# Optimization experiments

Hardware: AMD Instinct MI355X
Metric: run time of the kernel (lower is better)

## Reference

```python
import jax, jax.numpy as jnp
import numpy as np

TAU = 1.0   # temperature
BETA = 1.0  # instance_alingment_weight


def setup_inputs() -> dict:
    key = jax.random.key(0)
    k1, k2, k3 = jax.random.split(key, 3)
    N, D = 1024, 128
    return {
        "x": jax.random.normal(k1, (N, D), dtype=jnp.float32),
        "aug_x": jax.random.normal(k2, (N, D), dtype=jnp.float32),
        "label_prompt_embedding": jax.random.normal(k3, (N, D), dtype=jnp.float32),
    }


def _pair_loss(x, y, scale):
    # positive distances: ||x_i - y_i|| / (tau * sqrt(D)), shape [N]
    pos = jnp.linalg.norm(x - y, axis=1) * scale
    # pairwise distance matrix [N, N] via broadcasted [N, N, D] diff (as original)
    dm = jnp.linalg.norm(x[:, None, :] - y[None, :, :], axis=-1) * scale
    denom = jnp.sum(jnp.exp(dm), axis=1)  # [N]
    # log(exp(pos) / denom) == pos - log(denom)
    return jnp.mean(pos - jnp.log(denom))


def reference(x, aug_x, label_prompt_embedding):
    D = x.shape[-1]
    scale = 1.0 / (TAU * np.sqrt(D).astype(np.float32))
    center_alignment_loss = _pair_loss(x, label_prompt_embedding, scale)
    instance_alignment_loss = _pair_loss(x, aug_x, scale)
    alignment_loss = center_alignment_loss + BETA * instance_alignment_loss
    return (alignment_loss, center_alignment_loss, instance_alignment_loss)
```

## Files before the change

### kernel.cpp

```cpp
#include <hip/hip_runtime.h>
#include <math.h>

#define NN 1024
#define DD 128
#define JCH 8

typedef __bf16 bf16x8 __attribute__((ext_vector_type(8)));
typedef float  floatx4 __attribute__((ext_vector_type(4)));

#define WS_NORMS  786432
#define WS_DENOM  798720
#define WS_POS    864256

__global__ __launch_bounds__(256) void align_prep(
    const float* __restrict__ x, const float* __restrict__ lp,
    const float* __restrict__ aug, __bf16* __restrict__ mats,
    float* __restrict__ norms)
{
    const int w    = threadIdx.x >> 6;
    const int lane = threadIdx.x & 63;
    const int gw   = blockIdx.x * 4 + w;
    const int a    = gw >> 10;
    const int r    = gw & 1023;
    const float* src = (a == 0 ? x : (a == 1 ? lp : aug)) + (size_t)r * DD + lane * 2;
    const float2 v = *(const float2*)src;
    float sq = v.x * v.x + v.y * v.y;
    union { __bf16 b[2]; unsigned u; } t;
    t.b[0] = (__bf16)v.x; t.b[1] = (__bf16)v.y;
    *(unsigned*)(mats + (size_t)a * (NN * DD) + (size_t)r * DD + lane * 2) = t.u;
#pragma unroll
    for (int m = 1; m < 64; m <<= 1) sq += __shfl_xor(sq, m);
    if (lane == 0) norms[a * NN + r] = sq;
}

__global__ __launch_bounds__(256) void align_pair_kernel(
    const __bf16* __restrict__ mats, const float* __restrict__ norms,
    float* __restrict__ denom_part, float* __restrict__ posbuf)
{
    const float SCALE = 0.08838834764831845f;
    const int bx = blockIdx.x;
    const int p  = blockIdx.y;
    const int jc = blockIdx.z;
    const __bf16* __restrict__ A = mats;
    const __bf16* __restrict__ B = mats + (size_t)(p ? 2 : 1) * (NN * DD);
    const float*  __restrict__ nx = norms;
    const float*  __restrict__ ny = norms + (p ? 2 : 1) * NN;

    const int i0   = bx * 16;
    const int tid  = threadIdx.x;
    const int w    = tid >> 6;
    const int lane = tid & 63;
    const int col  = lane & 15;
    const int quad = lane >> 4;

    const __bf16* arow = A + (size_t)(i0 + col) * DD + quad * 8;
    bf16x8 afrag[4];
#pragma unroll
    for (int c = 0; c < 4; ++c) afrag[c] = *(const bf16x8*)(arow + c * 32);
    const float4 nxr = *(const float4*)(nx + i0 + quad * 4);

    float denom[4] = {0.f, 0.f, 0.f, 0.f};
    float pos[4]   = {0.f, 0.f, 0.f, 0.f};

#pragma unroll
    for (int t = 0; t < 2; ++t) {
        const int j0 = jc * 128 + t * 64 + w * 16;
        const __bf16* brow = B + (size_t)(j0 + col) * DD + quad * 8;
        bf16x8 bfrag[4];
#pragma unroll
        for (int c = 0; c < 4; ++c) bfrag[c] = *(const bf16x8*)(brow + c * 32);
        const float nyv = ny[j0 + col];

        floatx4 acc = {0.f, 0.f, 0.f, 0.f};
#pragma unroll
        for (int c = 0; c < 4; ++c)
            acc = __builtin_amdgcn_mfma_f32_16x16x32_bf16(afrag[c], bfrag[c], acc, 0, 0, 0);

#pragma unroll
        for (int r = 0; r < 4; ++r) {
            const int row = quad * 4 + r;
            float d2 = fmaf(-2.f, acc[r], nxr[r] + nyv);
            d2 = fmaxf(d2, 0.f);
            const float dm = SCALE * sqrtf(d2);
            denom[r] += __expf(dm);
            if (j0 + col == i0 + row) pos[r] = dm;
        }
    }

#pragma unroll
    for (int r = 0; r < 4; ++r) {
#pragma unroll
        for (int m = 1; m < 16; m <<= 1) {
            denom[r] += __shfl_xor(denom[r], m);
            pos[r]   += __shfl_xor(pos[r], m);
        }
    }

    __shared__ float ld_den[4][16];
    __shared__ float ld_pos[4][16];
    if (col == 0) {
#pragma unroll
        for (int r = 0; r < 4; ++r) {
            ld_den[w][quad * 4 + r] = denom[r];
            ld_pos[w][quad * 4 + r] = pos[r];
        }
    }
    __syncthreads();
    if (tid < 16) {
        const float den = ld_den[0][tid] + ld_den[1][tid] + ld_den[2][tid] + ld_den[3][tid];
        denom_part[(size_t)(p * JCH + jc) * NN + i0 + tid] = den;
        if (jc == (bx >> 3)) {
            const float po = ld_pos[0][tid] + ld_pos[1][tid] + ld_pos[2][tid] + ld_pos[3][tid];
            posbuf[p * NN + i0 + tid] = po;
        }
    }
}

__global__ __launch_bounds__(1024) void align_finalize(
    const float* __restrict__ denom_part, const float* __restrict__ posbuf,
    float* __restrict__ out)
{
    const int tid  = threadIdx.x;
    const int w    = tid >> 6;
    const int lane = tid & 63;
    float contrib[2];
#pragma unroll
    for (int p = 0; p < 2; ++p) {
        float den = 0.f;
#pragma unroll
        for (int jc = 0; jc < JCH; ++jc)
            den += denom_part[(size_t)(p * JCH + jc) * NN + tid];
        contrib[p] = posbuf[p * NN + tid] - __logf(den);
    }
    float c0 = contrib[0], c1 = contrib[1];
#pragma unroll
    for (int m = 1; m < 64; m <<= 1) {
        c0 += __shfl_xor(c0, m);
        c1 += __shfl_xor(c1, m);
    }
    __shared__ float s0[16], s1[16];
    if (lane == 0) { s0[w] = c0; s1[w] = c1; }
    __syncthreads();
    if (tid == 0) {
        float a = 0.f, b = 0.f;
#pragma unroll
        for (int k = 0; k < 16; ++k) { a += s0[k]; b += s1[k]; }
        const float inv = 1.0f / (float)NN;
        const float c  = a * inv;
        const float ia = b * inv;
        out[0] = c + ia;
        out[1] = c;
        out[2] = ia;
    }
}

extern "C" void kernel_launch(void* const* d_in, const int* in_sizes, int n_in,
                              void* d_out, int out_size, void* d_ws, size_t ws_size,
                              hipStream_t stream) {
    const float* x   = (const float*)d_in[0];
    const float* aug = (const float*)d_in[1];
    const float* lp  = (const float*)d_in[2];
    float* out       = (float*)d_out;

    char* ws = (char*)d_ws;
    __bf16* mats      = (__bf16*)ws;
    float*  norms     = (float*)(ws + WS_NORMS);
    float*  denom_par = (float*)(ws + WS_DENOM);
    float*  posbuf    = (float*)(ws + WS_POS);

    align_prep<<<768, 256, 0, stream>>>(x, lp, aug, mats, norms);
    align_pair_kernel<<<dim3(64, 2, JCH), 256, 0, stream>>>(mats, norms, denom_par, posbuf);
    align_finalize<<<1, 1024, 0, stream>>>(denom_par, posbuf, out);
}
```

Before: 68.32 us.

## Fuse finalize into pair kernel with atomic accumulation and last-block reduction

```diff
diff --git a/kernel.cpp b/kernel.cpp
--- a/kernel.cpp
+++ b/kernel.cpp
@@ -3,20 +3,20 @@
 
 #define NN 1024
 #define DD 128
-#define JCH 8
 
 typedef __bf16 bf16x8 __attribute__((ext_vector_type(8)));
 typedef float  floatx4 __attribute__((ext_vector_type(4)));
 
 #define WS_NORMS  786432
-#define WS_DENOM  798720
-#define WS_POS    864256
+#define WS_ACC    798720
 
 __global__ __launch_bounds__(256) void align_prep(
     const float* __restrict__ x, const float* __restrict__ lp,
     const float* __restrict__ aug, __bf16* __restrict__ mats,
-    float* __restrict__ norms)
+    float* __restrict__ norms, float* __restrict__ acc)
 {
+    if (blockIdx.x == 0 && threadIdx.x < 3) acc[threadIdx.x] = 0.0f;
+
     const int w    = threadIdx.x >> 6;
     const int lane = threadIdx.x & 63;
     const int gw   = blockIdx.x * 4 + w;
@@ -33,14 +33,13 @@
     if (lane == 0) norms[a * NN + r] = sq;
 }
 
-__global__ __launch_bounds__(256) void align_pair_kernel(
+__global__ __launch_bounds__(512) void align_pair_fused(
     const __bf16* __restrict__ mats, const float* __restrict__ norms,
-    float* __restrict__ denom_part, float* __restrict__ posbuf)
+    float* __restrict__ acc, float* __restrict__ out)
 {
     const float SCALE = 0.08838834764831845f;
     const int bx = blockIdx.x;
     const int p  = blockIdx.y;
-    const int jc = blockIdx.z;
     const __bf16* __restrict__ A = mats;
     const __bf16* __restrict__ B = mats + (size_t)(p ? 2 : 1) * (NN * DD);
     const float*  __restrict__ nx = norms;
@@ -62,24 +61,24 @@
     float denom[4] = {0.f, 0.f, 0.f, 0.f};
     float pos[4]   = {0.f, 0.f, 0.f, 0.f};
 
-#pragma unroll
-    for (int t = 0; t < 2; ++t) {
-        const int j0 = jc * 128 + t * 64 + w * 16;
+#pragma unroll 2
+    for (int jt = 0; jt < 8; ++jt) {
+        const int j0 = jt * 128 + w * 16;
         const __bf16* brow = B + (size_t)(j0 + col) * DD + quad * 8;
         bf16x8 bfrag[4];
 #pragma unroll
         for (int c = 0; c < 4; ++c) bfrag[c] = *(const bf16x8*)(brow + c * 32);
         const float nyv = ny[j0 + col];
 
-        floatx4 acc = {0.f, 0.f, 0.f, 0.f};
+        floatx4 acc4 = {0.f, 0.f, 0.f, 0.f};
 #pragma unroll
         for (int c = 0; c < 4; ++c)
-            acc = __builtin_amdgcn_mfma_f32_16x16x32_bf16(afrag[c], bfrag[c], acc, 0, 0, 0);
+            acc4 = __builtin_amdgcn_mfma_f32_16x16x32_bf16(afrag[c], bfrag[c], acc4, 0, 0, 0);
 
 #pragma unroll
         for (int r = 0; r < 4; ++r) {
             const int row = quad * 4 + r;
-            float d2 = fmaf(-2.f, acc[r], nxr[r] + nyv);
+            float d2 = fmaf(-2.f, acc4[r], nxr[r] + nyv);
             d2 = fmaxf(d2, 0.f);
             const float dm = SCALE * sqrtf(d2);
             denom[r] += __expf(dm);
@@ -96,8 +95,8 @@
         }
     }
 
-    __shared__ float ld_den[4][16];
-    __shared__ float ld_pos[4][16];
+    __shared__ float ld_den[8][16];
+    __shared__ float ld_pos[8][16];
     if (col == 0) {
 #pragma unroll
         for (int r = 0; r < 4; ++r) {
@@ -106,51 +105,32 @@
         }
     }
     __syncthreads();
+
+    float contrib = 0.f;
     if (tid < 16) {
-        const float den = ld_den[0][tid] + ld_den[1][tid] + ld_den[2][tid] + ld_den[3][tid];
-        denom_part[(size_t)(p * JCH + jc) * NN + i0 + tid] = den;
-        if (jc == (bx >> 3)) {
-            const float po = ld_pos[0][tid] + ld_pos[1][tid] + ld_pos[2][tid] + ld_pos[3][tid];
-            posbuf[p * NN + i0 + tid] = po;
+        float den = 0.f, po = 0.f;
+#pragma unroll
+        for (int k = 0; k < 8; ++k) { den += ld_den[k][tid]; po += ld_pos[k][tid]; }
+        contrib = po - __logf(den);
+    }
+    if (w == 0) {
+#pragma unroll
+        for (int m = 1; m < 16; m <<= 1) contrib += __shfl_xor(contrib, m);
+    }
+    if (tid == 0) {
+        atomicAdd(&acc[p], contrib);
+        __threadfence();
+        const unsigned old = atomicAdd((unsigned*)(acc + 2), 1u);
+        if (old == 127u) {
+            const float a  = atomicAdd(&acc[0], 0.0f);
+            const float b  = atomicAdd(&acc[1], 0.0f);
+            const float inv = 1.0f / (float)NN;
+            const float c  = a * inv;
+            const float ia = b * inv;
+            out[0] = c + ia;
+            out[1] = c;
+            out[2] = ia;
         }
-    }
-}
-
-__global__ __launch_bounds__(1024) void align_finalize(
-    const float* __restrict__ denom_part, const float* __restrict__ posbuf,
-    float* __restrict__ out)
-{
-    const int tid  = threadIdx.x;
-    const int w    = tid >> 6;
-    const int lane = tid & 63;
-    float contrib[2];
-#pragma unroll
-    for (int p = 0; p < 2; ++p) {
-        float den = 0.f;
-#pragma unroll
-        for (int jc = 0; jc < JCH; ++jc)
-            den += denom_part[(size_t)(p * JCH + jc) * NN + tid];
-        contrib[p] = posbuf[p * NN + tid] - __logf(den);
-    }
-    float c0 = contrib[0], c1 = contrib[1];
-#pragma unroll
-    for (int m = 1; m < 64; m <<= 1) {
-        c0 += __shfl_xor(c0, m);
-        c1 += __shfl_xor(c1, m);
-    }
-    __shared__ float s0[16], s1[16];
-    if (lane == 0) { s0[w] = c0; s1[w] = c1; }
-    __syncthreads();
-    if (tid == 0) {
-        float a = 0.f, b = 0.f;
-#pragma unroll
-        for (int k = 0; k < 16; ++k) { a += s0[k]; b += s1[k]; }
-        const float inv = 1.0f / (float)NN;
-        const float c  = a * inv;
-        const float ia = b * inv;
-        out[0] = c + ia;
-        out[1] = c;
-        out[2] = ia;
     }
 }
 
@@ -163,12 +143,10 @@
     float* out       = (float*)d_out;
 
     char* ws = (char*)d_ws;
-    __bf16* mats      = (__bf16*)ws;
-    float*  norms     = (float*)(ws + WS_NORMS);
-    float*  denom_par = (float*)(ws + WS_DENOM);
-    float*  posbuf    = (float*)(ws + WS_POS);
+    __bf16* mats  = (__bf16*)ws;
+    float*  norms = (float*)(ws + WS_NORMS);
+    float*  acc   = (float*)(ws + WS_ACC);
 
-    align_prep<<<768, 256, 0, stream>>>(x, lp, aug, mats, norms);
-    align_pair_kernel<<<dim3(64, 2, JCH), 256, 0, stream>>>(mats, norms, denom_par, posbuf);
-    align_finalize<<<1, 1024, 0, stream>>>(denom_par, posbuf, out);
+    align_prep<<<768, 256, 0, stream>>>(x, lp, aug, mats, norms, acc);
+    align_pair_fused<<<dim3(64, 2), 512, 0, stream>>>(mats, norms, acc, out);
 }
```

After: 71.36 us. 4.4% more time.
